# Optimization experiments

Hardware: AMD Instinct MI355X
Metric: run time of the kernel (lower is better)

The kernel has to match this reference:

```python
import jax, jax.numpy as jnp
import numpy as np

LEAKY_SLOPE = 0.2  # PyG GATConv default negative_slope
EPS = 1e-16


def _gat_layer(h_in, src, dst, W, a_src, a_dst, b, concat):
    # h_in: [N, Fin]; src/dst: [Etot] (self-loops included); W: [Fin, H*C]
    N = h_in.shape[0]
    H, C = a_src.shape
    h = (h_in @ W).reshape(N, H, C)                       # [N,H,C]
    al_s = jnp.sum(h * a_src, axis=-1)                    # [N,H]
    al_d = jnp.sum(h * a_dst, axis=-1)                    # [N,H]
    e = jax.nn.leaky_relu(al_s[src] + al_d[dst], LEAKY_SLOPE)  # [E,H]
    emax = jax.ops.segment_max(e, dst, num_segments=N)    # segment softmax over dst
    p = jnp.exp(e - emax[dst])
    denom = jax.ops.segment_sum(p, dst, num_segments=N)
    alpha = p / (denom[dst] + EPS)                        # [E,H]
    out = jax.ops.segment_sum(h[src] * alpha[:, :, None], dst, num_segments=N)  # [N,H,C]
    out = out.reshape(N, H * C) if concat else out.mean(axis=1)
    return out + b


def setup_inputs() -> dict:
    key = jax.random.key(0)
    ks = jax.random.split(key, 16)
    N, E, Fin, Hd, Hh = 10000, 320000, 256, 128, 4

    def glorot(k, shape, fan_in):
        return jax.random.normal(k, shape, dtype=jnp.float32) * (1.0 / np.sqrt(fan_in))

    inp = {
        "x": jax.random.normal(ks[0], (N, Fin), dtype=jnp.float32),
        "edge_index": jax.random.randint(ks[1], (2, E), 0, N, dtype=jnp.int32),
        # conv1: Fin -> Hd x Hh heads, concat
        "W1": glorot(ks[2], (Fin, Hh * Hd), Fin),
        "a1_src": glorot(ks[3], (Hh, Hd), Hd),
        "a1_dst": glorot(ks[4], (Hh, Hd), Hd),
        "b1": jnp.zeros((Hh * Hd,), jnp.float32),
        # conv2: Hh*Hd -> Hd x Hh heads, concat
        "W2": glorot(ks[5], (Hh * Hd, Hh * Hd), Hh * Hd),
        "a2_src": glorot(ks[6], (Hh, Hd), Hd),
        "a2_dst": glorot(ks[7], (Hh, Hd), Hd),
        "b2": jnp.zeros((Hh * Hd,), jnp.float32),
        # conv3: Hh*Hd -> Hd, 1 head, concat=False (mean)
        "W3": glorot(ks[8], (Hh * Hd, Hd), Hh * Hd),
        "a3_src": glorot(ks[9], (1, Hd), Hd),
        "a3_dst": glorot(ks[10], (1, Hd), Hd),
        "b3": jnp.zeros((Hd,), jnp.float32),
        # classifier: Hd -> Hd//2 -> 2
        "Wc1": glorot(ks[11], (Hd, Hd // 2), Hd),
        "bc1": jnp.zeros((Hd // 2,), jnp.float32),
        "Wc2": glorot(ks[12], (Hd // 2, 2), Hd // 2),
        "bc2": jnp.zeros((2,), jnp.float32),
    }
    return inp


def reference(x, edge_index, W1, a1_src, a1_dst, b1, W2, a2_src, a2_dst, b2,
              W3, a3_src, a3_dst, b3, Wc1, bc1, Wc2, bc2):
    N = x.shape[0]
    loops = jnp.arange(N, dtype=edge_index.dtype)
    src = jnp.concatenate([edge_index[0], loops])  # PyG adds self-loops
    dst = jnp.concatenate([edge_index[1], loops])

    h = jax.nn.elu(_gat_layer(x, src, dst, W1, a1_src, a1_dst, b1, concat=True))
    h = jax.nn.elu(_gat_layer(h, src, dst, W2, a2_src, a2_dst, b2, concat=True))
    embeddings = _gat_layer(h, src, dst, W3, a3_src, a3_dst, b3, concat=False)  # [N, 128]
    out = jax.nn.relu(embeddings @ Wc1 + bc1) @ Wc2 + bc2  # [N, 2]
    return out, embeddings
```

## Files before the change

kernel.cpp:

```cpp
#include <hip/hip_runtime.h>
#include <cstddef>

#define LEAKY 0.2f
#define EPS_DEN 1e-16f

typedef short bf8_t __attribute__((ext_vector_type(8)));
typedef float f4_t __attribute__((ext_vector_type(4)));
typedef unsigned short us4_t __attribute__((ext_vector_type(4)));
typedef unsigned short us8_t __attribute__((ext_vector_type(8)));

__device__ __forceinline__ unsigned short f2bf(float f) {
    unsigned u = __float_as_uint(f);
    unsigned r = (u + 0x7fffu + ((u >> 16) & 1u)) >> 16;
    return (unsigned short)r;
}
__device__ __forceinline__ float bf2f(unsigned short h) {
    return __uint_as_float(((unsigned)h) << 16);
}

__global__ void hist_kernel(const int* __restrict__ dst, int* __restrict__ counts, int E) {
    int i = blockIdx.x * blockDim.x + threadIdx.x;
    if (i < E) atomicAdd(&counts[dst[i]], 1);
}

__global__ void scan1_kernel(int* __restrict__ cnt, int* __restrict__ bsum, int N) {
    __shared__ int s[256];
    int t = threadIdx.x;
    int i = blockIdx.x * 256 + t;
    int v = (i < N) ? cnt[i] : 0;
    s[t] = v;
    __syncthreads();
#pragma unroll
    for (int st = 1; st < 256; st <<= 1) {
        int add = (t >= st) ? s[t - st] : 0;
        __syncthreads();
        s[t] += add;
        __syncthreads();
    }
    if (i < N) cnt[i] = s[t] - v;
    if (t == 255) bsum[blockIdx.x] = s[255];
}

__global__ void scan2_kernel(int* __restrict__ bsum, int* __restrict__ offs, int NB, int N) {
    int t = threadIdx.x;
    int v = (t < NB) ? bsum[t] : 0;
    int inc = v;
#pragma unroll
    for (int off = 1; off < 64; off <<= 1) {
        int u = __shfl_up(inc, off);
        if (t >= off) inc += u;
    }
    if (t < NB) bsum[t] = inc - v;
    if (t == 63) offs[N] = inc;
}

__global__ void scan3_kernel(int* __restrict__ cnt, const int* __restrict__ bsum,
                             int* __restrict__ offs, int N) {
    int i = blockIdx.x * 256 + threadIdx.x;
    if (i < N) {
        int o = cnt[i] + bsum[blockIdx.x];
        offs[i] = o;
        cnt[i] = o;
    }
}

__global__ void scatter_kernel(const int* __restrict__ src, const int* __restrict__ dst,
                               int* __restrict__ cursor, int* __restrict__ csrc, int E) {
    int i = blockIdx.x * blockDim.x + threadIdx.x;
    if (i < E) {
        int d = dst[i];
        int pos = atomicAdd(&cursor[d], 1);
        csrc[pos] = src[i];
    }
}

__global__ void split_kernel(const float* __restrict__ in, unsigned short* __restrict__ hi,
                             unsigned short* __restrict__ lo, int len) {
    int i = blockIdx.x * blockDim.x + threadIdx.x;
    if (i >= len) return;
    float v = in[i];
    unsigned short h = f2bf(v);
    hi[i] = h;
    lo[i] = f2bf(v - bf2f(h));
}

__global__ void wsplit_kernel(const float* __restrict__ W, unsigned short* __restrict__ hi,
                              unsigned short* __restrict__ lo, int K, int N) {
    int idx = blockIdx.x * blockDim.x + threadIdx.x;
    if (idx >= K * N) return;
    int n = idx / K, k = idx % K;
    float v = W[(size_t)k * N + n];
    unsigned short h = f2bf(v);
    hi[idx] = h;
    lo[idx] = f2bf(v - bf2f(h));
}

__global__ __launch_bounds__(256) void mfma_gemm128_kernel(
    const unsigned short* __restrict__ Ahi, const unsigned short* __restrict__ Alo,
    const unsigned short* __restrict__ BThi, const unsigned short* __restrict__ BTlo,
    float* __restrict__ C, int M, int N, int K) {
    constexpr int BK = 32;
    __shared__ __align__(16) unsigned short sAh[128 * BK];
    __shared__ __align__(16) unsigned short sAl[128 * BK];
    __shared__ __align__(16) unsigned short sBh[128 * BK];
    __shared__ __align__(16) unsigned short sBl[128 * BK];
    int t = threadIdx.x;
    int w = t >> 6, lane = t & 63;
    int quad = lane >> 4, low = lane & 15;
    int m0 = blockIdx.y * 128, n0 = blockIdx.x * 128;
    int wm = (w & 1) * 64, wn = (w >> 1) * 64;

    f4_t acc[4][4];
#pragma unroll
    for (int i = 0; i < 4; i++)
#pragma unroll
        for (int j = 0; j < 4; j++) acc[i][j] = (f4_t){0.f, 0.f, 0.f, 0.f};

    int srow = lane >> 2;
    int schunk = lane & 3;

    for (int k0 = 0; k0 < K; k0 += BK) {
        __syncthreads();
#pragma unroll
        for (int inst = 0; inst < 2; inst++) {
            int r = w * 32 + inst * 16 + srow;
            int gm = m0 + r;
            if (gm >= M) gm = M - 1;
            size_t goff = (size_t)gm * K + k0 + schunk * 8;
            size_t loff = (size_t)(w * 2048 + inst * 1024);
            __builtin_amdgcn_global_load_lds(
                (const __attribute__((address_space(1))) void*)(Ahi + goff),
                (__attribute__((address_space(3))) void*)((char*)sAh + loff), 16, 0, 0);
            __builtin_amdgcn_global_load_lds(
                (const __attribute__((address_space(1))) void*)(Alo + goff),
                (__attribute__((address_space(3))) void*)((char*)sAl + loff), 16, 0, 0);
        }
#pragma unroll
        for (int inst = 0; inst < 2; inst++) {
            int r = w * 32 + inst * 16 + srow;
            int gn = n0 + r;
            size_t goff = (size_t)gn * K + k0 + schunk * 8;
            size_t loff = (size_t)(w * 2048 + inst * 1024);
            __builtin_amdgcn_global_load_lds(
                (const __attribute__((address_space(1))) void*)(BThi + goff),
                (__attribute__((address_space(3))) void*)((char*)sBh + loff), 16, 0, 0);
            __builtin_amdgcn_global_load_lds(
                (const __attribute__((address_space(1))) void*)(BTlo + goff),
                (__attribute__((address_space(3))) void*)((char*)sBl + loff), 16, 0, 0);
        }
        __syncthreads();

        bf8_t afh[4], bfh[4], x[4];
#pragma unroll
        for (int i = 0; i < 4; i++) {
            int row = wm + i * 16 + low;
            afh[i] = *(const bf8_t*)&sAh[row * BK + quad * 8];
        }
#pragma unroll
        for (int j = 0; j < 4; j++) {
            int row = wn + j * 16 + low;
            bfh[j] = *(const bf8_t*)&sBh[row * BK + quad * 8];
        }
#pragma unroll
        for (int i = 0; i < 4; i++)
#pragma unroll
            for (int j = 0; j < 4; j++)
                acc[i][j] = __builtin_amdgcn_mfma_f32_16x16x32_bf16(afh[i], bfh[j], acc[i][j], 0, 0, 0);
#pragma unroll
        for (int j = 0; j < 4; j++) {
            int row = wn + j * 16 + low;
            x[j] = *(const bf8_t*)&sBl[row * BK + quad * 8];
        }
#pragma unroll
        for (int i = 0; i < 4; i++)
#pragma unroll
            for (int j = 0; j < 4; j++)
                acc[i][j] = __builtin_amdgcn_mfma_f32_16x16x32_bf16(afh[i], x[j], acc[i][j], 0, 0, 0);
#pragma unroll
        for (int i = 0; i < 4; i++) {
            int row = wm + i * 16 + low;
            x[i] = *(const bf8_t*)&sAl[row * BK + quad * 8];
        }
#pragma unroll
        for (int i = 0; i < 4; i++)
#pragma unroll
            for (int j = 0; j < 4; j++)
                acc[i][j] = __builtin_amdgcn_mfma_f32_16x16x32_bf16(x[i], bfh[j], acc[i][j], 0, 0, 0);
    }

#pragma unroll
    for (int i = 0; i < 4; i++) {
#pragma unroll
        for (int r = 0; r < 4; r++) {
            int gm = m0 + wm + i * 16 + quad * 4 + r;
            if (gm >= M) continue;
#pragma unroll
            for (int j = 0; j < 4; j++) {
                int gn = n0 + wn + j * 16 + low;
                C[(size_t)gm * N + gn] = acc[i][j][r];
            }
        }
    }
}

__global__ __launch_bounds__(256) void mfma_gemm64_kernel(
    const unsigned short* __restrict__ Ahi, const unsigned short* __restrict__ Alo,
    const unsigned short* __restrict__ BThi, const unsigned short* __restrict__ BTlo,
    float* __restrict__ C, int M, int N, int K) {
    constexpr int BK = 32;
    __shared__ __align__(16) unsigned short sAh[64 * BK];
    __shared__ __align__(16) unsigned short sAl[64 * BK];
    __shared__ __align__(16) unsigned short sBh[128 * BK];
    __shared__ __align__(16) unsigned short sBl[128 * BK];
    int t = threadIdx.x;
    int w = t >> 6, lane = t & 63;
    int quad = lane >> 4, low = lane & 15;
    int m0 = blockIdx.y * 64, n0 = blockIdx.x * 128;
    int wm = (w & 1) * 32, wn = (w >> 1) * 64;

    f4_t acc[2][4];
#pragma unroll
    for (int i = 0; i < 2; i++)
#pragma unroll
        for (int j = 0; j < 4; j++) acc[i][j] = (f4_t){0.f, 0.f, 0.f, 0.f};

    int srow = lane >> 2;
    int schunk = lane & 3;

    for (int k0 = 0; k0 < K; k0 += BK) {
        __syncthreads();
        {
            int gm = m0 + w * 16 + srow;
            if (gm >= M) gm = M - 1;
            size_t goff = (size_t)gm * K + k0 + schunk * 8;
            size_t loff = (size_t)(w * 1024);
            __builtin_amdgcn_global_load_lds(
                (const __attribute__((address_space(1))) void*)(Ahi + goff),
                (__attribute__((address_space(3))) void*)((char*)sAh + loff), 16, 0, 0);
            __builtin_amdgcn_global_load_lds(
                (const __attribute__((address_space(1))) void*)(Alo + goff),
                (__attribute__((address_space(3))) void*)((char*)sAl + loff), 16, 0, 0);
        }
#pragma unroll
        for (int inst = 0; inst < 2; inst++) {
            int gn = n0 + w * 32 + inst * 16 + srow;
            size_t goff = (size_t)gn * K + k0 + schunk * 8;
            size_t loff = (size_t)(w * 2048 + inst * 1024);
            __builtin_amdgcn_global_load_lds(
                (const __attribute__((address_space(1))) void*)(BThi + goff),
                (__attribute__((address_space(3))) void*)((char*)sBh + loff), 16, 0, 0);
            __builtin_amdgcn_global_load_lds(
                (const __attribute__((address_space(1))) void*)(BTlo + goff),
                (__attribute__((address_space(3))) void*)((char*)sBl + loff), 16, 0, 0);
        }
        __syncthreads();

        bf8_t afh[2], bfh[4], x[4];
#pragma unroll
        for (int i = 0; i < 2; i++) {
            int row = wm + i * 16 + low;
            afh[i] = *(const bf8_t*)&sAh[row * BK + quad * 8];
        }
#pragma unroll
        for (int j = 0; j < 4; j++) {
            int row = wn + j * 16 + low;
            bfh[j] = *(const bf8_t*)&sBh[row * BK + quad * 8];
        }
#pragma unroll
        for (int i = 0; i < 2; i++)
#pragma unroll
            for (int j = 0; j < 4; j++)
                acc[i][j] = __builtin_amdgcn_mfma_f32_16x16x32_bf16(afh[i], bfh[j], acc[i][j], 0, 0, 0);
#pragma unroll
        for (int j = 0; j < 4; j++) {
            int row = wn + j * 16 + low;
            x[j] = *(const bf8_t*)&sBl[row * BK + quad * 8];
        }
#pragma unroll
        for (int i = 0; i < 2; i++)
#pragma unroll
            for (int j = 0; j < 4; j++)
                acc[i][j] = __builtin_amdgcn_mfma_f32_16x16x32_bf16(afh[i], x[j], acc[i][j], 0, 0, 0);
#pragma unroll
        for (int i = 0; i < 2; i++) {
            int row = wm + i * 16 + low;
            x[i] = *(const bf8_t*)&sAl[row * BK + quad * 8];
        }
#pragma unroll
        for (int i = 0; i < 2; i++)
#pragma unroll
            for (int j = 0; j < 4; j++)
                acc[i][j] = __builtin_amdgcn_mfma_f32_16x16x32_bf16(x[i], bfh[j], acc[i][j], 0, 0, 0);
    }

#pragma unroll
    for (int i = 0; i < 2; i++) {
#pragma unroll
        for (int r = 0; r < 4; r++) {
            int gm = m0 + wm + i * 16 + quad * 4 + r;
            if (gm >= M) continue;
#pragma unroll
            for (int j = 0; j < 4; j++) {
                int gn = n0 + wn + j * 16 + low;
                C[(size_t)gm * N + gn] = acc[i][j][r];
            }
        }
    }
}

__global__ void al_h4_kernel(const float* __restrict__ h, const float* __restrict__ a_src,
                             const float* __restrict__ a_dst, float* __restrict__ als,
                             float* __restrict__ ald, int N) {
    int wave = threadIdx.x >> 6, lane = threadIdx.x & 63;
    int n = blockIdx.x * 4 + wave;
    if (n >= N) return;
    const float* row = h + (size_t)n * 512;
    float ps[4] = {0, 0, 0, 0}, pd[4] = {0, 0, 0, 0};
#pragma unroll
    for (int k = 0; k < 8; k++) {
        int f = k * 64 + lane;
        float v = row[f];
        ps[k >> 1] += v * a_src[f];
        pd[k >> 1] += v * a_dst[f];
    }
#pragma unroll
    for (int off = 32; off; off >>= 1) {
#pragma unroll
        for (int hd = 0; hd < 4; hd++) {
            ps[hd] += __shfl_down(ps[hd], off);
            pd[hd] += __shfl_down(pd[hd], off);
        }
    }
    if (lane == 0) {
#pragma unroll
        for (int hd = 0; hd < 4; hd++) {
            als[n * 4 + hd] = ps[hd];
            ald[n * 4 + hd] = pd[hd];
        }
    }
}

__global__ void al_h1_kernel(const float* __restrict__ h, const float* __restrict__ a_src,
                             const float* __restrict__ a_dst, float* __restrict__ als,
                             float* __restrict__ ald, int N) {
    int wave = threadIdx.x >> 6, lane = threadIdx.x & 63;
    int n = blockIdx.x * 4 + wave;
    if (n >= N) return;
    const float* row = h + (size_t)n * 128;
    float v0 = row[lane], v1 = row[lane + 64];
    float ps = v0 * a_src[lane] + v1 * a_src[lane + 64];
    float pd = v0 * a_dst[lane] + v1 * a_dst[lane + 64];
#pragma unroll
    for (int off = 32; off; off >>= 1) {
        ps += __shfl_down(ps, off);
        pd += __shfl_down(pd, off);
    }
    if (lane == 0) { als[n] = ps; ald[n] = pd; }
}

__global__ void stats_h4_kernel(const int* __restrict__ csrc, const int* __restrict__ offs,
                                const float* __restrict__ als, const float* __restrict__ ald,
                                float* __restrict__ pbuf, float* __restrict__ psf,
                                float* __restrict__ rden, int N, int E) {
    int wave = threadIdx.x >> 6, lane = threadIdx.x & 63;
    int n = blockIdx.x * 4 + wave;
    if (n >= N) return;
    int hd = lane & 3, es = lane >> 2;
    float aldn = ald[n * 4 + hd];
    float selfe = als[n * 4 + hd] + aldn;
    selfe = selfe > 0.f ? selfe : LEAKY * selfe;
    int beg = offs[n], end = offs[n + 1];
    float* pb = pbuf + (size_t)hd * E;
    float m = selfe;
    for (int base = beg; base + es < end; base += 16) {
        int idx = base + es;
        int s = csrc[idx];
        float e = als[s * 4 + hd] + aldn;
        e = e > 0.f ? e : LEAKY * e;
        pb[idx] = e;
        m = fmaxf(m, e);
    }
#pragma unroll
    for (int off = 4; off < 64; off <<= 1) m = fmaxf(m, __shfl_xor(m, off));
    float d = 0.f;
    for (int base = beg; base + es < end; base += 16) {
        int idx = base + es;
        float p = __expf(pb[idx] - m);
        pb[idx] = p;
        d += p;
    }
#pragma unroll
    for (int off = 4; off < 64; off <<= 1) d += __shfl_xor(d, off);
    float pself = __expf(selfe - m);
    float r = 1.0f / (d + pself + EPS_DEN);
    if (es == 0) {
        psf[n * 4 + hd] = pself;
        rden[n * 4 + hd] = r;
    }
}

__global__ void stats_h1_kernel(const int* __restrict__ csrc, const int* __restrict__ offs,
                                const float* __restrict__ als, const float* __restrict__ ald,
                                float* __restrict__ pbuf, float* __restrict__ psf,
                                float* __restrict__ rden, int N) {
    int wave = threadIdx.x >> 6, lane = threadIdx.x & 63;
    int n = blockIdx.x * 4 + wave;
    if (n >= N) return;
    float aldn = ald[n];
    float selfe = als[n] + aldn;
    selfe = selfe > 0.f ? selfe : LEAKY * selfe;
    int beg = offs[n], end = offs[n + 1];
    float m = selfe;
    for (int base = beg; base + lane < end; base += 64) {
        int idx = base + lane;
        int s = csrc[idx];
        float e = als[s] + aldn;
        e = e > 0.f ? e : LEAKY * e;
        pbuf[idx] = e;
        m = fmaxf(m, e);
    }
#pragma unroll
    for (int off = 1; off < 64; off <<= 1) m = fmaxf(m, __shfl_xor(m, off));
    float d = 0.f;
    for (int base = beg; base + lane < end; base += 64) {
        int idx = base + lane;
        float p = __expf(pbuf[idx] - m);
        pbuf[idx] = p;
        d += p;
    }
#pragma unroll
    for (int off = 1; off < 64; off <<= 1) d += __shfl_xor(d, off);
    float pself = __expf(selfe - m);
    float r = 1.0f / (d + pself + EPS_DEN);
    if (lane == 0) { psf[n] = pself; rden[n] = r; }
}

template <bool DO_ELU>
__global__ __launch_bounds__(64) void gat_agg_hh_kernel(
    const float* __restrict__ h, const float* __restrict__ pbuf,
    const float* __restrict__ psf, const float* __restrict__ rden,
    const int* __restrict__ csrc, const int* __restrict__ offs,
    const float* __restrict__ bias, unsigned short* __restrict__ ohi,
    unsigned short* __restrict__ olo, int N, int E) {
    int gid = blockIdx.x;
    int hh = gid & 7;
    int n = gid >> 3;
    int head = hh >> 1;
    int lane = threadIdx.x;
    int eg = lane >> 3;
    int fl = (lane & 7) * 8;
    int f0 = hh * 64 + fl;
    const float* pb = pbuf + (size_t)head * E;
    int beg = offs[n], end = offs[n + 1];

    f4_t a0 = (f4_t){0.f, 0.f, 0.f, 0.f};
    f4_t a1 = (f4_t){0.f, 0.f, 0.f, 0.f};
#pragma unroll 2
    for (int c = beg + eg; c < end; c += 8) {
        int s = csrc[c];
        float p = pb[c];
        const float* srow = h + (size_t)s * 512 + f0;
        f4_t x0 = *(const f4_t*)(srow);
        f4_t x1 = *(const f4_t*)(srow + 4);
        a0 += p * x0;
        a1 += p * x1;
    }
    if (eg == 0) {
        float p = psf[n * 4 + head];
        const float* srow = h + (size_t)n * 512 + f0;
        a0 += p * *(const f4_t*)(srow);
        a1 += p * *(const f4_t*)(srow + 4);
    }
#pragma unroll
    for (int j = 0; j < 4; j++) {
        a0[j] += __shfl_xor(a0[j], 8);
        a0[j] += __shfl_xor(a0[j], 16);
        a0[j] += __shfl_xor(a0[j], 32);
        a1[j] += __shfl_xor(a1[j], 8);
        a1[j] += __shfl_xor(a1[j], 16);
        a1[j] += __shfl_xor(a1[j], 32);
    }
    if (lane < 8) {
        int fo = hh * 64 + lane * 8;
        float r = rden[n * 4 + head];
        f4_t b0 = *(const f4_t*)(bias + fo);
        f4_t b1 = *(const f4_t*)(bias + fo + 4);
        us8_t hs, ls;
#pragma unroll
        for (int j = 0; j < 4; j++) {
            float o = a0[j] * r + b0[j];
            if (DO_ELU) o = o > 0.f ? o : (__expf(o) - 1.0f);
            unsigned short hv = f2bf(o);
            hs[j] = hv;
            ls[j] = f2bf(o - bf2f(hv));
        }
#pragma unroll
        for (int j = 0; j < 4; j++) {
            float o = a1[j] * r + b1[j];
            if (DO_ELU) o = o > 0.f ? o : (__expf(o) - 1.0f);
            unsigned short hv = f2bf(o);
            hs[4 + j] = hv;
            ls[4 + j] = f2bf(o - bf2f(hv));
        }
        size_t idx = (size_t)n * 512 + fo;
        *(us8_t*)&ohi[idx] = hs;
        *(us8_t*)&olo[idx] = ls;
    }
}

__global__ __launch_bounds__(64) void gat_agg_h1_cls_kernel(
    const float* __restrict__ h, const float* __restrict__ pbuf,
    const float* __restrict__ psf, const float* __restrict__ rden,
    const int* __restrict__ csrc, const int* __restrict__ offs,
    const float* __restrict__ bias, const float* __restrict__ Wc1,
    const float* __restrict__ bc1, const float* __restrict__ Wc2,
    const float* __restrict__ bc2, float* __restrict__ emb,
    float* __restrict__ outp, int N) {
    int n = blockIdx.x;
    int lane = threadIdx.x;
    int eg = lane >> 4;
    int fl = (lane & 15) * 8;
    __shared__ float semb[128];
    int beg = offs[n], end = offs[n + 1];

    f4_t a0 = (f4_t){0.f, 0.f, 0.f, 0.f};
    f4_t a1 = (f4_t){0.f, 0.f, 0.f, 0.f};
#pragma unroll 2
    for (int c = beg + eg; c < end; c += 4) {
        int s = csrc[c];
        float p = pbuf[c];
        const float* srow = h + (size_t)s * 128 + fl;
        a0 += p * *(const f4_t*)(srow);
        a1 += p * *(const f4_t*)(srow + 4);
    }
    if (eg == 0) {
        float p = psf[n];
        const float* srow = h + (size_t)n * 128 + fl;
        a0 += p * *(const f4_t*)(srow);
        a1 += p * *(const f4_t*)(srow + 4);
    }
#pragma unroll
    for (int j = 0; j < 4; j++) {
        a0[j] += __shfl_xor(a0[j], 16);
        a0[j] += __shfl_xor(a0[j], 32);
        a1[j] += __shfl_xor(a1[j], 16);
        a1[j] += __shfl_xor(a1[j], 32);
    }
    if (lane < 16) {
        int fo = lane * 8;
        float r = rden[n];
        f4_t b0 = *(const f4_t*)(bias + fo);
        f4_t b1 = *(const f4_t*)(bias + fo + 4);
        f4_t o0, o1;
#pragma unroll
        for (int j = 0; j < 4; j++) {
            o0[j] = a0[j] * r + b0[j];
            o1[j] = a1[j] * r + b1[j];
        }
        *(f4_t*)&semb[fo] = o0;
        *(f4_t*)&semb[fo + 4] = o1;
        *(f4_t*)&emb[(size_t)n * 128 + fo] = o0;
        *(f4_t*)&emb[(size_t)n * 128 + fo + 4] = o1;
    }
    __syncthreads();

    float cacc = bc1[lane];
#pragma unroll 4
    for (int k = 0; k < 128; k++) cacc += semb[k] * Wc1[k * 64 + lane];
    cacc = fmaxf(cacc, 0.f);
    float o0 = cacc * Wc2[lane * 2 + 0];
    float o1 = cacc * Wc2[lane * 2 + 1];
#pragma unroll
    for (int off = 32; off; off >>= 1) {
        o0 += __shfl_down(o0, off);
        o1 += __shfl_down(o1, off);
    }
    if (lane == 0) {
        outp[n * 2 + 0] = o0 + bc2[0];
        outp[n * 2 + 1] = o1 + bc2[1];
    }
}

extern "C" void kernel_launch(void* const* d_in, const int* in_sizes, int n_in,
                              void* d_out, int out_size, void* d_ws, size_t ws_size,
                              hipStream_t stream) {
    const float* x      = (const float*)d_in[0];
    const int*   ei     = (const int*)d_in[1];
    const float* W1     = (const float*)d_in[2];
    const float* a1s    = (const float*)d_in[3];
    const float* a1d    = (const float*)d_in[4];
    const float* b1     = (const float*)d_in[5];
    const float* W2     = (const float*)d_in[6];
    const float* a2s    = (const float*)d_in[7];
    const float* a2d    = (const float*)d_in[8];
    const float* b2     = (const float*)d_in[9];
    const float* W3     = (const float*)d_in[10];
    const float* a3s    = (const float*)d_in[11];
    const float* a3d    = (const float*)d_in[12];
    const float* b3     = (const float*)d_in[13];
    const float* Wc1    = (const float*)d_in[14];
    const float* bc1    = (const float*)d_in[15];
    const float* Wc2    = (const float*)d_in[16];
    const float* bc2    = (const float*)d_in[17];

    const int N = in_sizes[0] / 256;
    const int E = in_sizes[1] / 2;
    const int F = 512;

    const int* src = ei;
    const int* dst = ei + E;

    auto align = [](size_t o) { return (o + 255) & ~(size_t)255; };
    size_t o = 0;
    size_t o_G     = o; o = align(o + (size_t)N * F * 4);
    size_t o_ahi   = o; o = align(o + (size_t)N * F * 2);
    size_t o_alo   = o; o = align(o + (size_t)N * F * 2);
    size_t o_xhi   = o; o = align(o + (size_t)N * 256 * 2);
    size_t o_xlo   = o; o = align(o + (size_t)N * 256 * 2);
    size_t o_w1h   = o; o = align(o + (size_t)512 * 256 * 2);
    size_t o_w1l   = o; o = align(o + (size_t)512 * 256 * 2);
    size_t o_w2h   = o; o = align(o + (size_t)512 * 512 * 2);
    size_t o_w2l   = o; o = align(o + (size_t)512 * 512 * 2);
    size_t o_w3h   = o; o = align(o + (size_t)128 * 512 * 2);
    size_t o_w3l   = o; o = align(o + (size_t)128 * 512 * 2);
    size_t o_als   = o; o = align(o + (size_t)N * 4 * 4);
    size_t o_ald   = o; o = align(o + (size_t)N * 4 * 4);
    size_t o_psf   = o; o = align(o + (size_t)N * 4 * 4);
    size_t o_rden  = o; o = align(o + (size_t)N * 4 * 4);
    size_t o_cnt   = o; o = align(o + (size_t)N * 4);
    size_t o_off   = o; o = align(o + (size_t)(N + 1) * 4);
    size_t o_bsum  = o; o = align(o + (size_t)64 * 4);
    size_t o_csrc  = o; o = align(o + (size_t)E * 4);
    size_t o_ebuf  = o; o = align(o + (size_t)E * 4 * 4);
    (void)ws_size;

    char* ws = (char*)d_ws;
    float* bufG  = (float*)(ws + o_G);
    unsigned short* act_hi = (unsigned short*)(ws + o_ahi);
    unsigned short* act_lo = (unsigned short*)(ws + o_alo);
    unsigned short* x_hi   = (unsigned short*)(ws + o_xhi);
    unsigned short* x_lo   = (unsigned short*)(ws + o_xlo);
    unsigned short* w1h = (unsigned short*)(ws + o_w1h);
    unsigned short* w1l = (unsigned short*)(ws + o_w1l);
    unsigned short* w2h = (unsigned short*)(ws + o_w2h);
    unsigned short* w2l = (unsigned short*)(ws + o_w2l);
    unsigned short* w3h = (unsigned short*)(ws + o_w3h);
    unsigned short* w3l = (unsigned short*)(ws + o_w3l);
    float* als  = (float*)(ws + o_als);
    float* ald  = (float*)(ws + o_ald);
    float* psf  = (float*)(ws + o_psf);
    float* rden = (float*)(ws + o_rden);
    int*   cnt  = (int*)(ws + o_cnt);
    int*   offs = (int*)(ws + o_off);
    int*   bsum = (int*)(ws + o_bsum);
    int*   csrc = (int*)(ws + o_csrc);
    float* ebuf = (float*)(ws + o_ebuf);

    float* outp = (float*)d_out;
    float* emb  = (float*)d_out + (size_t)N * 2;

    hipMemsetAsync(cnt, 0, (size_t)N * 4, stream);
    int eb = (E + 255) / 256;
    int nbs = (N + 255) / 256;
    hipLaunchKernelGGL(hist_kernel, dim3(eb), dim3(256), 0, stream, dst, cnt, E);
    hipLaunchKernelGGL(scan1_kernel, dim3(nbs), dim3(256), 0, stream, cnt, bsum, N);
    hipLaunchKernelGGL(scan2_kernel, dim3(1), dim3(64), 0, stream, bsum, offs, nbs, N);
    hipLaunchKernelGGL(scan3_kernel, dim3(nbs), dim3(256), 0, stream, cnt, bsum, offs, N);
    hipLaunchKernelGGL(scatter_kernel, dim3(eb), dim3(256), 0, stream, src, dst, cnt, csrc, E);

    hipLaunchKernelGGL(split_kernel, dim3((N * 256 + 255) / 256), dim3(256), 0, stream,
                       x, x_hi, x_lo, N * 256);
    hipLaunchKernelGGL(wsplit_kernel, dim3((256 * 512 + 255) / 256), dim3(256), 0, stream,
                       W1, w1h, w1l, 256, 512);
    hipLaunchKernelGGL(wsplit_kernel, dim3((512 * 512 + 255) / 256), dim3(256), 0, stream,
                       W2, w2h, w2l, 512, 512);
    hipLaunchKernelGGL(wsplit_kernel, dim3((512 * 128 + 255) / 256), dim3(256), 0, stream,
                       W3, w3h, w3l, 512, 128);

    int nb4 = (N + 3) / 4;
    int gy128 = (N + 127) / 128;
    int gy64  = (N + 63) / 64;

    hipLaunchKernelGGL(mfma_gemm128_kernel, dim3(512 / 128, gy128), dim3(256), 0, stream,
                       x_hi, x_lo, w1h, w1l, bufG, N, 512, 256);
    hipLaunchKernelGGL(al_h4_kernel, dim3(nb4), dim3(256), 0, stream, bufG, a1s, a1d, als, ald, N);
    hipLaunchKernelGGL(stats_h4_kernel, dim3(nb4), dim3(256), 0, stream,
                       csrc, offs, als, ald, ebuf, psf, rden, N, E);
    hipLaunchKernelGGL((gat_agg_hh_kernel<true>), dim3(N * 8), dim3(64), 0, stream,
                       bufG, ebuf, psf, rden, csrc, offs, b1, act_hi, act_lo, N, E);

    hipLaunchKernelGGL(mfma_gemm128_kernel, dim3(512 / 128, gy128), dim3(256), 0, stream,
                       act_hi, act_lo, w2h, w2l, bufG, N, 512, 512);
    hipLaunchKernelGGL(al_h4_kernel, dim3(nb4), dim3(256), 0, stream, bufG, a2s, a2d, als, ald, N);
    hipLaunchKernelGGL(stats_h4_kernel, dim3(nb4), dim3(256), 0, stream,
                       csrc, offs, als, ald, ebuf, psf, rden, N, E);
    hipLaunchKernelGGL((gat_agg_hh_kernel<true>), dim3(N * 8), dim3(64), 0, stream,
                       bufG, ebuf, psf, rden, csrc, offs, b2, act_hi, act_lo, N, E);

    hipLaunchKernelGGL(mfma_gemm64_kernel, dim3(128 / 128, gy64), dim3(256), 0, stream,
                       act_hi, act_lo, w3h, w3l, bufG, N, 128, 512);
    hipLaunchKernelGGL(al_h1_kernel, dim3(nb4), dim3(256), 0, stream, bufG, a3s, a3d, als, ald, N);
    hipLaunchKernelGGL(stats_h1_kernel, dim3(nb4), dim3(256), 0, stream,
                       csrc, offs, als, ald, ebuf, psf, rden, N);
    hipLaunchKernelGGL(gat_agg_h1_cls_kernel, dim3(N), dim3(64), 0, stream,
                       bufG, ebuf, psf, rden, csrc, offs, b3, Wc1, bc1, Wc2, bc2, emb, outp, N);
}
```

Baseline: 383.5 us.

## Fuse attention logits into GEMM epilogue, merge split/scan kernels, stage edges in LDS

```diff
diff --git a/kernel.cpp b/kernel.cpp
--- a/kernel.cpp
+++ b/kernel.cpp
@@ -41,27 +41,30 @@
     if (t == 255) bsum[blockIdx.x] = s[255];
 }
 
-__global__ void scan2_kernel(int* __restrict__ bsum, int* __restrict__ offs, int NB, int N) {
+__global__ void scan3b_kernel(int* __restrict__ cnt, const int* __restrict__ bsum,
+                              int* __restrict__ offs, int N, int NB) {
+    __shared__ int sPre[64];
+    __shared__ int sTot;
     int t = threadIdx.x;
-    int v = (t < NB) ? bsum[t] : 0;
-    int inc = v;
-#pragma unroll
-    for (int off = 1; off < 64; off <<= 1) {
-        int u = __shfl_up(inc, off);
-        if (t >= off) inc += u;
-    }
-    if (t < NB) bsum[t] = inc - v;
-    if (t == 63) offs[N] = inc;
-}
-
-__global__ void scan3_kernel(int* __restrict__ cnt, const int* __restrict__ bsum,
-                             int* __restrict__ offs, int N) {
-    int i = blockIdx.x * 256 + threadIdx.x;
+    if (t < 64) {
+        int v = (t < NB) ? bsum[t] : 0;
+        int inc = v;
+#pragma unroll
+        for (int off = 1; off < 64; off <<= 1) {
+            int u = __shfl_up(inc, off);
+            if (t >= off) inc += u;
+        }
+        sPre[t] = inc - v;
+        if (t == 63) sTot = inc;
+    }
+    __syncthreads();
+    int i = blockIdx.x * 256 + t;
     if (i < N) {
-        int o = cnt[i] + bsum[blockIdx.x];
+        int o = cnt[i] + sPre[blockIdx.x];
         offs[i] = o;
         cnt[i] = o;
     }
+    if (blockIdx.x == 0 && t == 0) offs[N] = sTot;
 }
 
 __global__ void scatter_kernel(const int* __restrict__ src, const int* __restrict__ dst,
@@ -74,36 +77,55 @@
     }
 }
 
-__global__ void split_kernel(const float* __restrict__ in, unsigned short* __restrict__ hi,
-                             unsigned short* __restrict__ lo, int len) {
-    int i = blockIdx.x * blockDim.x + threadIdx.x;
-    if (i >= len) return;
-    float v = in[i];
-    unsigned short h = f2bf(v);
-    hi[i] = h;
-    lo[i] = f2bf(v - bf2f(h));
-}
-
-__global__ void wsplit_kernel(const float* __restrict__ W, unsigned short* __restrict__ hi,
-                              unsigned short* __restrict__ lo, int K, int N) {
-    int idx = blockIdx.x * blockDim.x + threadIdx.x;
-    if (idx >= K * N) return;
-    int n = idx / K, k = idx % K;
-    float v = W[(size_t)k * N + n];
-    unsigned short h = f2bf(v);
-    hi[idx] = h;
-    lo[idx] = f2bf(v - bf2f(h));
+__global__ void split_all_kernel(
+    const float* __restrict__ x, unsigned short* __restrict__ xh, unsigned short* __restrict__ xl,
+    int NBX,
+    const float* __restrict__ W1, unsigned short* __restrict__ w1h, unsigned short* __restrict__ w1l,
+    const float* __restrict__ W2, unsigned short* __restrict__ w2h, unsigned short* __restrict__ w2l,
+    const float* __restrict__ W3, unsigned short* __restrict__ w3h, unsigned short* __restrict__ w3l) {
+    int b = blockIdx.x, t = threadIdx.x;
+    float v;
+    unsigned short* ph;
+    unsigned short* pl;
+    int idx;
+    if (b < NBX) {
+        idx = b * 256 + t;
+        v = x[idx];
+        ph = xh; pl = xl;
+    } else if (b < NBX + 512) {
+        idx = (b - NBX) * 256 + t;
+        int n = idx >> 8, k = idx & 255;
+        v = W1[(size_t)k * 512 + n];
+        ph = w1h; pl = w1l;
+    } else if (b < NBX + 512 + 1024) {
+        idx = (b - NBX - 512) * 256 + t;
+        int n = idx >> 9, k = idx & 511;
+        v = W2[(size_t)k * 512 + n];
+        ph = w2h; pl = w2l;
+    } else {
+        idx = (b - NBX - 1536) * 256 + t;
+        int n = idx >> 9, k = idx & 511;
+        v = W3[(size_t)k * 128 + n];
+        ph = w3h; pl = w3l;
+    }
+    unsigned short hv = f2bf(v);
+    ph[idx] = hv;
+    pl[idx] = f2bf(v - bf2f(hv));
 }
 
 __global__ __launch_bounds__(256) void mfma_gemm128_kernel(
     const unsigned short* __restrict__ Ahi, const unsigned short* __restrict__ Alo,
     const unsigned short* __restrict__ BThi, const unsigned short* __restrict__ BTlo,
-    float* __restrict__ C, int M, int N, int K) {
+    const float* __restrict__ a_src, const float* __restrict__ a_dst,
+    float* __restrict__ C, float* __restrict__ als, float* __restrict__ ald,
+    int M, int N, int K) {
     constexpr int BK = 32;
     __shared__ __align__(16) unsigned short sAh[128 * BK];
     __shared__ __align__(16) unsigned short sAl[128 * BK];
     __shared__ __align__(16) unsigned short sBh[128 * BK];
     __shared__ __align__(16) unsigned short sBl[128 * BK];
+    __shared__ float sAls[128][2];
+    __shared__ float sAld[128][2];
     int t = threadIdx.x;
     int w = t >> 6, lane = t & 63;
     int quad = lane >> 4, low = lane & 15;
@@ -150,7 +172,7 @@
         }
         __syncthreads();
 
-        bf8_t afh[4], bfh[4], x[4];
+        bf8_t afh[4], bfh[4], xx[4];
 #pragma unroll
         for (int i = 0; i < 4; i++) {
             int row = wm + i * 16 + low;
@@ -169,23 +191,23 @@
 #pragma unroll
         for (int j = 0; j < 4; j++) {
             int row = wn + j * 16 + low;
-            x[j] = *(const bf8_t*)&sBl[row * BK + quad * 8];
+            xx[j] = *(const bf8_t*)&sBl[row * BK + quad * 8];
         }
 #pragma unroll
         for (int i = 0; i < 4; i++)
 #pragma unroll
             for (int j = 0; j < 4; j++)
-                acc[i][j] = __builtin_amdgcn_mfma_f32_16x16x32_bf16(afh[i], x[j], acc[i][j], 0, 0, 0);
+                acc[i][j] = __builtin_amdgcn_mfma_f32_16x16x32_bf16(afh[i], xx[j], acc[i][j], 0, 0, 0);
 #pragma unroll
         for (int i = 0; i < 4; i++) {
             int row = wm + i * 16 + low;
-            x[i] = *(const bf8_t*)&sAl[row * BK + quad * 8];
+            xx[i] = *(const bf8_t*)&sAl[row * BK + quad * 8];
         }
 #pragma unroll
         for (int i = 0; i < 4; i++)
 #pragma unroll
             for (int j = 0; j < 4; j++)
-                acc[i][j] = __builtin_amdgcn_mfma_f32_16x16x32_bf16(x[i], bfh[j], acc[i][j], 0, 0, 0);
+                acc[i][j] = __builtin_amdgcn_mfma_f32_16x16x32_bf16(xx[i], bfh[j], acc[i][j], 0, 0, 0);
     }
 
 #pragma unroll
@@ -201,17 +223,59 @@
             }
         }
     }
+
+    int hd = n0 >> 7;
+    float as_[4], ad_[4];
+#pragma unroll
+    for (int j = 0; j < 4; j++) {
+        int c = wn + j * 16 + low;
+        as_[j] = a_src[hd * 128 + c];
+        ad_[j] = a_dst[hd * 128 + c];
+    }
+    int chh = wn >> 6;
+#pragma unroll
+    for (int i = 0; i < 4; i++) {
+#pragma unroll
+        for (int r = 0; r < 4; r++) {
+            float v = acc[i][0][r] * as_[0] + acc[i][1][r] * as_[1] +
+                      acc[i][2][r] * as_[2] + acc[i][3][r] * as_[3];
+            float vd = acc[i][0][r] * ad_[0] + acc[i][1][r] * ad_[1] +
+                       acc[i][2][r] * ad_[2] + acc[i][3][r] * ad_[3];
+#pragma unroll
+            for (int off = 1; off < 16; off <<= 1) {
+                v += __shfl_xor(v, off);
+                vd += __shfl_xor(vd, off);
+            }
+            if (low == 0) {
+                int row = wm + i * 16 + quad * 4 + r;
+                sAls[row][chh] = v;
+                sAld[row][chh] = vd;
+            }
+        }
+    }
+    __syncthreads();
+    if (t < 128) {
+        int gm = m0 + t;
+        if (gm < M) {
+            als[gm * 4 + hd] = sAls[t][0] + sAls[t][1];
+            ald[gm * 4 + hd] = sAld[t][0] + sAld[t][1];
+        }
+    }
 }
 
 __global__ __launch_bounds__(256) void mfma_gemm64_kernel(
     const unsigned short* __restrict__ Ahi, const unsigned short* __restrict__ Alo,
     const unsigned short* __restrict__ BThi, const unsigned short* __restrict__ BTlo,
-    float* __restrict__ C, int M, int N, int K) {
+    const float* __restrict__ a_src, const float* __restrict__ a_dst,
+    float* __restrict__ C, float* __restrict__ als, float* __restrict__ ald,
+    int M, int N, int K) {
     constexpr int BK = 32;
     __shared__ __align__(16) unsigned short sAh[64 * BK];
     __shared__ __align__(16) unsigned short sAl[64 * BK];
     __shared__ __align__(16) unsigned short sBh[128 * BK];
     __shared__ __align__(16) unsigned short sBl[128 * BK];
+    __shared__ float sAls[64][2];
+    __shared__ float sAld[64][2];
     int t = threadIdx.x;
     int w = t >> 6, lane = t & 63;
     int quad = lane >> 4, low = lane & 15;
@@ -255,7 +319,7 @@
         }
         __syncthreads();
 
-        bf8_t afh[2], bfh[4], x[4];
+        bf8_t afh[2], bfh[4], xx[4];
 #pragma unroll
         for (int i = 0; i < 2; i++) {
             int row = wm + i * 16 + low;
@@ -274,23 +338,23 @@
 #pragma unroll
         for (int j = 0; j < 4; j++) {
             int row = wn + j * 16 + low;
-            x[j] = *(const bf8_t*)&sBl[row * BK + quad * 8];
+            xx[j] = *(const bf8_t*)&sBl[row * BK + quad * 8];
         }
 #pragma unroll
         for (int i = 0; i < 2; i++)
 #pragma unroll
             for (int j = 0; j < 4; j++)
-                acc[i][j] = __builtin_amdgcn_mfma_f32_16x16x32_bf16(afh[i], x[j], acc[i][j], 0, 0, 0);
+                acc[i][j] = __builtin_amdgcn_mfma_f32_16x16x32_bf16(afh[i], xx[j], acc[i][j], 0, 0, 0);
 #pragma unroll
         for (int i = 0; i < 2; i++) {
             int row = wm + i * 16 + low;
-            x[i] = *(const bf8_t*)&sAl[row * BK + quad * 8];
+            xx[i] = *(const bf8_t*)&sAl[row * BK + quad * 8];
         }
 #pragma unroll
         for (int i = 0; i < 2; i++)
 #pragma unroll
             for (int j = 0; j < 4; j++)
-                acc[i][j] = __builtin_amdgcn_mfma_f32_16x16x32_bf16(x[i], bfh[j], acc[i][j], 0, 0, 0);
+                acc[i][j] = __builtin_amdgcn_mfma_f32_16x16x32_bf16(xx[i], bfh[j], acc[i][j], 0, 0, 0);
     }
 
 #pragma unroll
@@ -306,56 +370,43 @@
             }
         }
     }
-}
-
-__global__ void al_h4_kernel(const float* __restrict__ h, const float* __restrict__ a_src,
-                             const float* __restrict__ a_dst, float* __restrict__ als,
-                             float* __restrict__ ald, int N) {
-    int wave = threadIdx.x >> 6, lane = threadIdx.x & 63;
-    int n = blockIdx.x * 4 + wave;
-    if (n >= N) return;
-    const float* row = h + (size_t)n * 512;
-    float ps[4] = {0, 0, 0, 0}, pd[4] = {0, 0, 0, 0};
-#pragma unroll
-    for (int k = 0; k < 8; k++) {
-        int f = k * 64 + lane;
-        float v = row[f];
-        ps[k >> 1] += v * a_src[f];
-        pd[k >> 1] += v * a_dst[f];
-    }
-#pragma unroll
-    for (int off = 32; off; off >>= 1) {
-#pragma unroll
-        for (int hd = 0; hd < 4; hd++) {
-            ps[hd] += __shfl_down(ps[hd], off);
-            pd[hd] += __shfl_down(pd[hd], off);
-        }
-    }
-    if (lane == 0) {
-#pragma unroll
-        for (int hd = 0; hd < 4; hd++) {
-            als[n * 4 + hd] = ps[hd];
-            ald[n * 4 + hd] = pd[hd];
-        }
-    }
-}
-
-__global__ void al_h1_kernel(const float* __restrict__ h, const float* __restrict__ a_src,
-                             const float* __restrict__ a_dst, float* __restrict__ als,
-                             float* __restrict__ ald, int N) {
-    int wave = threadIdx.x >> 6, lane = threadIdx.x & 63;
-    int n = blockIdx.x * 4 + wave;
-    if (n >= N) return;
-    const float* row = h + (size_t)n * 128;
-    float v0 = row[lane], v1 = row[lane + 64];
-    float ps = v0 * a_src[lane] + v1 * a_src[lane + 64];
-    float pd = v0 * a_dst[lane] + v1 * a_dst[lane + 64];
-#pragma unroll
-    for (int off = 32; off; off >>= 1) {
-        ps += __shfl_down(ps, off);
-        pd += __shfl_down(pd, off);
-    }
-    if (lane == 0) { als[n] = ps; ald[n] = pd; }
+
+    float as_[4], ad_[4];
+#pragma unroll
+    for (int j = 0; j < 4; j++) {
+        int c = wn + j * 16 + low;
+        as_[j] = a_src[c];
+        ad_[j] = a_dst[c];
+    }
+    int chh = wn >> 6;
+#pragma unroll
+    for (int i = 0; i < 2; i++) {
+#pragma unroll
+        for (int r = 0; r < 4; r++) {
+            float v = acc[i][0][r] * as_[0] + acc[i][1][r] * as_[1] +
+                      acc[i][2][r] * as_[2] + acc[i][3][r] * as_[3];
+            float vd = acc[i][0][r] * ad_[0] + acc[i][1][r] * ad_[1] +
+                       acc[i][2][r] * ad_[2] + acc[i][3][r] * ad_[3];
+#pragma unroll
+            for (int off = 1; off < 16; off <<= 1) {
+                v += __shfl_xor(v, off);
+                vd += __shfl_xor(vd, off);
+            }
+            if (low == 0) {
+                int row = wm + i * 16 + quad * 4 + r;
+                sAls[row][chh] = v;
+                sAld[row][chh] = vd;
+            }
+        }
+    }
+    __syncthreads();
+    if (t < 64) {
+        int gm = m0 + t;
+        if (gm < M) {
+            als[gm] = sAls[t][0] + sAls[t][1];
+            ald[gm] = sAld[t][0] + sAld[t][1];
+        }
+    }
 }
 
 __global__ void stats_h4_kernel(const int* __restrict__ csrc, const int* __restrict__ offs,
@@ -447,64 +498,60 @@
     int n = gid >> 3;
     int head = hh >> 1;
     int lane = threadIdx.x;
-    int eg = lane >> 3;
-    int fl = (lane & 7) * 8;
-    int f0 = hh * 64 + fl;
+    int eg = lane >> 4;
+    int f0 = hh * 64 + (lane & 15) * 4;
     const float* pb = pbuf + (size_t)head * E;
+
+    __shared__ int   sSrc[2][64];
+    __shared__ float sP[2][64];
     int beg = offs[n], end = offs[n + 1];
-
-    f4_t a0 = (f4_t){0.f, 0.f, 0.f, 0.f};
-    f4_t a1 = (f4_t){0.f, 0.f, 0.f, 0.f};
-#pragma unroll 2
-    for (int c = beg + eg; c < end; c += 8) {
-        int s = csrc[c];
-        float p = pb[c];
-        const float* srow = h + (size_t)s * 512 + f0;
-        f4_t x0 = *(const f4_t*)(srow);
-        f4_t x1 = *(const f4_t*)(srow + 4);
-        a0 += p * x0;
-        a1 += p * x1;
+    int nchunks = (end - beg + 63) >> 6;
+
+    f4_t acc = (f4_t){0.f, 0.f, 0.f, 0.f};
+    if (beg + lane < end) {
+        sSrc[0][lane] = csrc[beg + lane] << 9;
+        sP[0][lane] = pb[beg + lane];
+    }
+    for (int ch = 0; ch < nchunks; ch++) {
+        int base = beg + ch * 64;
+        int len = min(64, end - base);
+        int buf = ch & 1;
+        __syncthreads();
+        int nbase = base + 64;
+        if (ch + 1 < nchunks && nbase + lane < end) {
+            sSrc[buf ^ 1][lane] = csrc[nbase + lane] << 9;
+            sP[buf ^ 1][lane] = pb[nbase + lane];
+        }
+#pragma unroll 8
+        for (int c = eg; c < len; c += 4) {
+            const float* srow = h + (size_t)(unsigned)sSrc[buf][c] + f0;
+            acc += sP[buf][c] * *(const f4_t*)srow;
+        }
     }
     if (eg == 0) {
-        float p = psf[n * 4 + head];
-        const float* srow = h + (size_t)n * 512 + f0;
-        a0 += p * *(const f4_t*)(srow);
-        a1 += p * *(const f4_t*)(srow + 4);
+        f4_t x = *(const f4_t*)(h + (size_t)n * 512 + f0);
+        acc += psf[n * 4 + head] * x;
     }
 #pragma unroll
     for (int j = 0; j < 4; j++) {
-        a0[j] += __shfl_xor(a0[j], 8);
-        a0[j] += __shfl_xor(a0[j], 16);
-        a0[j] += __shfl_xor(a0[j], 32);
-        a1[j] += __shfl_xor(a1[j], 8);
-        a1[j] += __shfl_xor(a1[j], 16);
-        a1[j] += __shfl_xor(a1[j], 32);
-    }
-    if (lane < 8) {
-        int fo = hh * 64 + lane * 8;
+        acc[j] += __shfl_xor(acc[j], 16);
+        acc[j] += __shfl_xor(acc[j], 32);
+    }
+    if (lane < 16) {
         float r = rden[n * 4 + head];
-        f4_t b0 = *(const f4_t*)(bias + fo);
-        f4_t b1 = *(const f4_t*)(bias + fo + 4);
-        us8_t hs, ls;
+        f4_t b = *(const f4_t*)(bias + f0);
+        us4_t hs, ls;
 #pragma unroll
         for (int j = 0; j < 4; j++) {
-            float o = a0[j] * r + b0[j];
+            float o = acc[j] * r + b[j];
             if (DO_ELU) o = o > 0.f ? o : (__expf(o) - 1.0f);
             unsigned short hv = f2bf(o);
             hs[j] = hv;
             ls[j] = f2bf(o - bf2f(hv));
         }
-#pragma unroll
-        for (int j = 0; j < 4; j++) {
-            float o = a1[j] * r + b1[j];
-            if (DO_ELU) o = o > 0.f ? o : (__expf(o) - 1.0f);
-            unsigned short hv = f2bf(o);
-            hs[4 + j] = hv;
-            ls[4 + j] = f2bf(o - bf2f(hv));
-        }
-        size_t idx = (size_t)n * 512 + fo;
-        *(us8_t*)&ohi[idx] = hs;
-        *(us8_t*)&olo[idx] = ls;
+        size_t idx = (size_t)n * 512 + f0;
+        *(us4_t*)&ohi[idx] = hs;
+        *(us4_t*)&olo[idx] = ls;
     }
 }
 
@@ -520,18 +567,35 @@
     int lane = threadIdx.x;
     int eg = lane >> 4;
     int fl = (lane & 15) * 8;
+    __shared__ int   sSrc[2][64];
+    __shared__ float sP[2][64];
     __shared__ float semb[128];
     int beg = offs[n], end = offs[n + 1];
+    int nchunks = (end - beg + 63) >> 6;
 
     f4_t a0 = (f4_t){0.f, 0.f, 0.f, 0.f};
     f4_t a1 = (f4_t){0.f, 0.f, 0.f, 0.f};
-#pragma unroll 2
-    for (int c = beg + eg; c < end; c += 4) {
-        int s = csrc[c];
-        float p = pbuf[c];
-        const float* srow = h + (size_t)s * 128 + fl;
-        a0 += p * *(const f4_t*)(srow);
-        a1 += p * *(const f4_t*)(srow + 4);
+    if (beg + lane < end) {
+        sSrc[0][lane] = csrc[beg + lane] << 7;
+        sP[0][lane] = pbuf[beg + lane];
+    }
+    for (int ch = 0; ch < nchunks; ch++) {
+        int base = beg + ch * 64;
+        int len = min(64, end - base);
+        int buf = ch & 1;
+        __syncthreads();
+        int nbase = base + 64;
+        if (ch + 1 < nchunks && nbase + lane < end) {
+            sSrc[buf ^ 1][lane] = csrc[nbase + lane] << 7;
+            sP[buf ^ 1][lane] = pbuf[nbase + lane];
+        }
+#pragma unroll 8
+        for (int c = eg; c < len; c += 4) {
+            const float* srow = h + (size_t)(unsigned)sSrc[buf][c] + fl;
+            float p = sP[buf][c];
+            a0 += p * *(const f4_t*)(srow);
+            a1 += p * *(const f4_t*)(srow + 4);
+        }
     }
     if (eg == 0) {
         float p = psf[n];
@@ -546,6 +610,7 @@
         a1[j] += __shfl_xor(a1[j], 16);
         a1[j] += __shfl_xor(a1[j], 32);
     }
+    __syncthreads();
     if (lane < 16) {
         int fo = lane * 8;
         float r = rden[n];
@@ -664,42 +729,33 @@
     int nbs = (N + 255) / 256;
     hipLaunchKernelGGL(hist_kernel, dim3(eb), dim3(256), 0, stream, dst, cnt, E);
     hipLaunchKernelGGL(scan1_kernel, dim3(nbs), dim3(256), 0, stream, cnt, bsum, N);
-    hipLaunchKernelGGL(scan2_kernel, dim3(1), dim3(64), 0, stream, bsum, offs, nbs, N);
-    hipLaunchKernelGGL(scan3_kernel, dim3(nbs), dim3(256), 0, stream, cnt, bsum, offs, N);
+    hipLaunchKernelGGL(scan3b_kernel, dim3(nbs), dim3(256), 0, stream, cnt, bsum, offs, N, nbs);
     hipLaunchKernelGGL(scatter_kernel, dim3(eb), dim3(256), 0, stream, src, dst, cnt, csrc, E);
 
-    hipLaunchKernelGGL(split_kernel, dim3((N * 256 + 255) / 256), dim3(256), 0, stream,
-                       x, x_hi, x_lo, N * 256);
-    hipLaunchKernelGGL(wsplit_kernel, dim3((256 * 512 + 255) / 256), dim3(256), 0, stream,
-                       W1, w1h, w1l, 256, 512);
-    hipLaunchKernelGGL(wsplit_kernel, dim3((512 * 512 + 255) / 256), dim3(256), 0, stream,
-                       W2, w2h, w2l, 512, 512);
-    hipLaunchKernelGGL(wsplit_kernel, dim3((512 * 128 + 255) / 256), dim3(256), 0, stream,
-                       W3, w3h, w3l, 512, 128);
+    int NBX = N;
+    hipLaunchKernelGGL(split_all_kernel, dim3(NBX + 512 + 1024 + 256), dim3(256), 0, stream,
+                       x, x_hi, x_lo, NBX, W1, w1h, w1l, W2, w2h, w2l, W3, w3h, w3l);
 
     int nb4 = (N + 3) / 4;
     int gy128 = (N + 127) / 128;
     int gy64  = (N + 63) / 64;
 
     hipLaunchKernelGGL(mfma_gemm128_kernel, dim3(512 / 128, gy128), dim3(256), 0, stream,
-                       x_hi, x_lo, w1h, w1l, bufG, N, 512, 256);
-    hipLaunchKernelGGL(al_h4_kernel, dim3(nb4), dim3(256), 0, stream, bufG, a1s, a1d, als, ald, N);
+                       x_hi, x_lo, w1h, w1l, a1s, a1d, bufG, als, ald, N, 512, 256);
     hipLaunchKernelGGL(stats_h4_kernel, dim3(nb4), dim3(256), 0, stream,
                        csrc, offs, als, ald, ebuf, psf, rden, N, E);
     hipLaunchKernelGGL((gat_agg_hh_kernel<true>), dim3(N * 8), dim3(64), 0, stream,
                        bufG, ebuf, psf, rden, csrc, offs, b1, act_hi, act_lo, N, E);
 
     hipLaunchKernelGGL(mfma_gemm128_kernel, dim3(512 / 128, gy128), dim3(256), 0, stream,
-                       act_hi, act_lo, w2h, w2l, bufG, N, 512, 512);
-    hipLaunchKernelGGL(al_h4_kernel, dim3(nb4), dim3(256), 0, stream, bufG, a2s, a2d, als, ald, N);
+                       act_hi, act_lo, w2h, w2l, a2s, a2d, bufG, als, ald, N, 512, 512);
     hipLaunchKernelGGL(stats_h4_kernel, dim3(nb4), dim3(256), 0, stream,
                        csrc, offs, als, ald, ebuf, psf, rden, N, E);
     hipLaunchKernelGGL((gat_agg_hh_kernel<true>), dim3(N * 8), dim3(64), 0, stream,
                        bufG, ebuf, psf, rden, csrc, offs, b2, act_hi, act_lo, N, E);
 
     hipLaunchKernelGGL(mfma_gemm64_kernel, dim3(128 / 128, gy64), dim3(256), 0, stream,
-                       act_hi, act_lo, w3h, w3l, bufG, N, 128, 512);
-    hipLaunchKernelGGL(al_h1_kernel, dim3(nb4), dim3(256), 0, stream, bufG, a3s, a3d, als, ald, N);
+                       act_hi, act_lo, w3h, w3l, a3s, a3d, bufG, als, ald, N, 128, 512);
     hipLaunchKernelGGL(stats_h1_kernel, dim3(nb4), dim3(256), 0, stream,
                        csrc, offs, als, ald, ebuf, psf, rden, N);
     hipLaunchKernelGGL(gat_agg_h1_cls_kernel, dim3(N), dim3(64), 0, stream,
```

Result: faster. 363.2 us (-5.3%).
